# Kernel tuning notes

Hardware: AMD Instinct MI355X
Metric: run time of the kernel (lower is better)

## Reference

```python
import jax, jax.numpy as jnp
import numpy as np

N = 100000      # nodes
E = 3200000     # edges (avg degree 32)
IN = 256        # in_features
OUT = 128       # out_features


def setup_inputs() -> dict:
    key = jax.random.key(0)
    k_x, k_r, k_c, k_v, k_w, k_b = jax.random.split(key, 6)
    x = jax.random.normal(k_x, (N, IN), dtype=jnp.float32)
    row = jax.random.randint(k_r, (E,), 0, N)          # destination node of each edge
    col = jax.random.randint(k_c, (E,), 0, N)          # source node of each edge
    adj_vals = jax.random.uniform(k_v, (E,), dtype=jnp.float32)  # sparse adj values
    stdv = 1.0 / np.sqrt(OUT)                          # matches reset_parameters
    weight = jax.random.uniform(k_w, (IN, OUT), dtype=jnp.float32, minval=-stdv, maxval=stdv)
    bias = jax.random.uniform(k_b, (OUT,), dtype=jnp.float32, minval=-stdv, maxval=stdv)
    return {"x": x, "adj_vals": adj_vals, "weight": weight, "bias": bias,
            "row": row, "col": col}


def reference(x, adj_vals, weight, bias, row, col):
    # support = input @ W                       [N, OUT]
    support = x @ weight
    # output = spmm(adj, support): for each edge (r, c, v): out[r] += v * support[c]
    gathered = adj_vals[:, None] * support[col]  # [E, OUT] irregular gather
    out = jax.ops.segment_sum(gathered, row, num_segments=N)  # [N, OUT] scatter-add
    return out + bias
```

## Files before the change

### kernel.cpp

```cpp
#include <hip/hip_runtime.h>

#define INF 256
#define OUTF 128
#define NBMAX 1024
#define BUCKET_CAP 4608

typedef _Float16 half2v __attribute__((ext_vector_type(2)));
typedef _Float16 half8 __attribute__((ext_vector_type(8)));
typedef float f32x4 __attribute__((ext_vector_type(4)));

__device__ inline unsigned short f16bits(float v) {
    union { unsigned short u; _Float16 h; } cv;
    cv.h = (_Float16)v;
    return cv.u;
}
__device__ inline float f16val15(unsigned rec) {
    union { unsigned short u; _Float16 h; } cv;
    cv.u = (unsigned short)(rec << 1);
    return (float)cv.h;
}

__global__ __launch_bounds__(256) void k_prepack(const float* __restrict__ w,
                                                 _Float16* __restrict__ wpack,
                                                 int* __restrict__ bcursor,
                                                 int NB) {
    int t = blockIdx.x * 256 + threadIdx.x;
    int k = t >> 7, n = t & 127;
    int ks = k >> 5, quad = (k >> 3) & 3, j = k & 7;
    int ct = n >> 4, nn = n & 15;
    wpack[(((ks * 8 + ct) * 4 + quad) * 16 + nn) * 8 + j] = (_Float16)w[k * OUTF + n];
    if (t < NB) bcursor[t] = t * BUCKET_CAP;
}

__global__ __launch_bounds__(256) void gcn_gemm_mfma(const float* __restrict__ x,
                                                     const _Float16* __restrict__ wpack,
                                                     _Float16* __restrict__ support,
                                                     int N) {
    const int tid = threadIdx.x;
    const int wv = tid >> 6;
    const int lane = tid & 63;
    const int m16 = lane & 15;
    const int quad = lane >> 4;
    const int rowbase = blockIdx.x * 128 + wv * 32;

    f32x4 acc[2][8];
#pragma unroll
    for (int rt = 0; rt < 2; ++rt)
#pragma unroll
        for (int ct = 0; ct < 8; ++ct)
            acc[rt][ct] = (f32x4){0.f, 0.f, 0.f, 0.f};

    int r0 = rowbase + m16;
    int r1 = rowbase + 16 + m16;
    int r0c = (r0 < N) ? r0 : N - 1;
    int r1c = (r1 < N) ? r1 : N - 1;
    const float* xr0 = x + (long)r0c * INF + quad * 8;
    const float* xr1 = x + (long)r1c * INF + quad * 8;

    for (int ks = 0; ks < 8; ++ks) {
        float4 u0 = *(const float4*)(xr0 + ks * 32);
        float4 v0 = *(const float4*)(xr0 + ks * 32 + 4);
        float4 u1 = *(const float4*)(xr1 + ks * 32);
        float4 v1 = *(const float4*)(xr1 + ks * 32 + 4);
        half8 a0 = {(_Float16)u0.x, (_Float16)u0.y, (_Float16)u0.z, (_Float16)u0.w,
                    (_Float16)v0.x, (_Float16)v0.y, (_Float16)v0.z, (_Float16)v0.w};
        half8 a1 = {(_Float16)u1.x, (_Float16)u1.y, (_Float16)u1.z, (_Float16)u1.w,
                    (_Float16)v1.x, (_Float16)v1.y, (_Float16)v1.z, (_Float16)v1.w};

        half8 b[8];
#pragma unroll
        for (int ct = 0; ct < 8; ++ct)
            b[ct] = *(const half8*)(wpack + (size_t)(((ks * 8 + ct) * 4 + quad) * 16 + m16) * 8);

#pragma unroll
        for (int ct = 0; ct < 8; ++ct) {
            acc[0][ct] = __builtin_amdgcn_mfma_f32_16x16x32_f16(a0, b[ct], acc[0][ct], 0, 0, 0);
            acc[1][ct] = __builtin_amdgcn_mfma_f32_16x16x32_f16(a1, b[ct], acc[1][ct], 0, 0, 0);
        }
    }

#pragma unroll
    for (int rt = 0; rt < 2; ++rt) {
        int rb = rowbase + rt * 16 + quad * 4;
#pragma unroll
        for (int reg = 0; reg < 4; ++reg) {
            int r = rb + reg;
            if (r < N) {
#pragma unroll
                for (int ct = 0; ct < 8; ++ct)
                    support[(long)r * OUTF + ct * 16 + m16] = (_Float16)acc[rt][ct][reg];
            }
        }
    }
}

__global__ __launch_bounds__(256) void k_coarse_scatter(const int* __restrict__ row,
                                                        const int* __restrict__ col,
                                                        const float* __restrict__ vals,
                                                        int* __restrict__ bcursor,
                                                        uint2* __restrict__ tmp,
                                                        int NB, int E) {
    __shared__ int cnt[NBMAX];
    __shared__ int sbase[NBMAX];
    const int tid = threadIdx.x;
    for (int i = tid; i < NB; i += 256) cnt[i] = 0;
    __syncthreads();

    int b[16], rk[16];
    uint2 rec[16];
    int base = blockIdx.x * 4096;
#pragma unroll
    for (int j = 0; j < 16; ++j) {
        int e = base + j * 256 + tid;
        if (e < E) {
            int r = row[e];
            int c = col[e];
            float v = vals[e];
            rec[j].x = ((unsigned)r << 15) | ((unsigned)f16bits(v) >> 1);
            rec[j].y = (unsigned)c;
            b[j] = r >> 7;
            rk[j] = atomicAdd(&cnt[b[j]], 1);
        } else {
            b[j] = -1;
        }
    }
    __syncthreads();
    for (int i = tid; i < NB; i += 256) {
        int c = cnt[i];
        if (c) sbase[i] = atomicAdd(&bcursor[i], c);
    }
    __syncthreads();
#pragma unroll
    for (int j = 0; j < 16; ++j) {
        if (b[j] >= 0) tmp[sbase[b[j]] + rk[j]] = rec[j];
    }
}

__global__ __launch_bounds__(256) void k_bucket_sort(const uint2* __restrict__ tmp,
                                                     const int* __restrict__ bcursor,
                                                     unsigned* __restrict__ frecs,
                                                     int* __restrict__ rs,
                                                     int* __restrict__ re,
                                                     int N) {
    __shared__ uint2 recs[BUCKET_CAP];
    __shared__ int cnt[128];
    __shared__ int offs[128];

    const int tid = threadIdx.x;
    const int b = blockIdx.x;
    const int start = b * BUCKET_CAP;
    int n = bcursor[b] - start;
    if (n > BUCKET_CAP) n = BUCKET_CAP;
    const int row0 = b << 7;

    if (tid < 128) cnt[tid] = 0;
    __syncthreads();

    for (int i = tid; i < n; i += 256) {
        uint2 r = tmp[start + i];
        recs[i] = r;
        atomicAdd(&cnt[(r.x >> 15) & 127], 1);
    }
    __syncthreads();

    if (tid < 128) offs[tid] = cnt[tid];
    __syncthreads();
    for (int d = 1; d < 128; d <<= 1) {
        int add = 0;
        if (tid < 128 && tid >= d) add = offs[tid - d];
        __syncthreads();
        if (tid < 128) offs[tid] += add;
        __syncthreads();
    }
    if (tid < 128) {
        int excl = offs[tid] - cnt[tid];
        offs[tid] = excl;
        int r = row0 + tid;
        if (r < N) {
            rs[r] = start + excl;
            re[r] = start + excl + cnt[tid];
        }
    }
    __syncthreads();

    for (int i = tid; i < n; i += 256) {
        uint2 r = recs[i];
        int lr = (r.x >> 15) & 127;
        int pos = atomicAdd(&offs[lr], 1);
        frecs[start + pos] = (r.y << 15) | (r.x & 0x7FFF);
    }
}

__global__ __launch_bounds__(256) void k_gather(const half2v* __restrict__ sup,
                                                const unsigned* __restrict__ frecs,
                                                const int* __restrict__ rs,
                                                const int* __restrict__ re,
                                                const float* __restrict__ bias,
                                                float* __restrict__ out,
                                                int N) {
    int wid = (blockIdx.x * 256 + threadIdx.x) >> 6;
    int lane = threadIdx.x & 63;
    if (wid >= N) return;

    int start = rs[wid];
    int end = re[wid];

    float ax = 0.f, ay = 0.f;
    int i = start;
    for (; i + 4 <= end; i += 4) {
        unsigned r0 = frecs[i + 0], r1 = frecs[i + 1];
        unsigned r2 = frecs[i + 2], r3 = frecs[i + 3];
        float v0 = f16val15(r0), v1 = f16val15(r1);
        float v2 = f16val15(r2), v3 = f16val15(r3);
        half2v h0 = sup[(long)(r0 >> 15) * 64 + lane];
        half2v h1 = sup[(long)(r1 >> 15) * 64 + lane];
        half2v h2 = sup[(long)(r2 >> 15) * 64 + lane];
        half2v h3 = sup[(long)(r3 >> 15) * 64 + lane];
        ax += v0 * (float)h0.x + v1 * (float)h1.x + v2 * (float)h2.x + v3 * (float)h3.x;
        ay += v0 * (float)h0.y + v1 * (float)h1.y + v2 * (float)h2.y + v3 * (float)h3.y;
    }
    for (; i < end; ++i) {
        unsigned r = frecs[i];
        float v = f16val15(r);
        half2v h = sup[(long)(r >> 15) * 64 + lane];
        ax += v * (float)h.x;
        ay += v * (float)h.y;
    }

    float2 bb = ((const float2*)bias)[lane];
    float2 o;
    o.x = ax + bb.x;
    o.y = ay + bb.y;
    ((float2*)out)[(long)wid * 64 + lane] = o;
}

extern "C" void kernel_launch(void* const* d_in, const int* in_sizes, int n_in,
                              void* d_out, int out_size, void* d_ws, size_t ws_size,
                              hipStream_t stream) {
    const float* x    = (const float*)d_in[0];
    const float* vals = (const float*)d_in[1];
    const float* w    = (const float*)d_in[2];
    const float* bias = (const float*)d_in[3];
    const int*   row  = (const int*)d_in[4];
    const int*   col  = (const int*)d_in[5];

    const int N = in_sizes[0] / INF;
    const int E = in_sizes[1];
    const int NB = (N + 127) / 128;

    char* p = (char*)d_ws;
    _Float16* support = (_Float16*)p;  p += (size_t)N * OUTF * sizeof(_Float16);
    unsigned* frecs   = (unsigned*)p;  p += (size_t)NB * BUCKET_CAP * sizeof(unsigned);
    _Float16* wpack   = (_Float16*)p;  p += (size_t)INF * OUTF * sizeof(_Float16);
    int* rs           = (int*)p;       p += (size_t)N * sizeof(int);
    int* re           = (int*)p;       p += (size_t)N * sizeof(int);
    int* bcursor      = (int*)p;       p += (size_t)NBMAX * sizeof(int);

    uint2* tmp = (uint2*)d_out;

    const int eb4096 = (E + 4095) / 4096;

    k_prepack<<<(INF * OUTF) / 256, 256, 0, stream>>>(w, wpack, bcursor, NB);

    gcn_gemm_mfma<<<(N + 127) / 128, 256, 0, stream>>>(x, wpack, support, N);

    k_coarse_scatter<<<eb4096, 256, 0, stream>>>(row, col, vals, bcursor, tmp, NB, E);

    k_bucket_sort<<<NB, 256, 0, stream>>>(tmp, bcursor, frecs, rs, re, N);

    {
        int blocks = (N * 64 + 255) / 256;
        k_gather<<<blocks, 256, 0, stream>>>((const half2v*)support, frecs,
                                             rs, re, bias, (float*)d_out, N);
    }
}
```

Before: 408.3 us.

## Merge GEMM and edge scatter into one launch, split-wave gather, drop LDS staging

The GEMM and the coarse edge scatter are independent, so they now run as disjoint block ranges of a single kernel and can overlap on the GPU instead of running back to back. The bucket sort no longer stages records in shared memory and instead re-reads them from global memory, which lowers LDS use and may raise occupancy at the cost of a second global read. The gather splits each wave into two halves that handle alternating edges. Each lane loads 4 halves per edge with vectorized record reads, and the halves are combined by a cross-lane shuffle, which is meant to raise memory-level parallelism.

```diff
diff --git a/kernel.cpp b/kernel.cpp
--- a/kernel.cpp
+++ b/kernel.cpp
@@ -6,6 +6,7 @@
 #define BUCKET_CAP 4608
 
 typedef _Float16 half2v __attribute__((ext_vector_type(2)));
+typedef _Float16 half4 __attribute__((ext_vector_type(4)));
 typedef _Float16 half8 __attribute__((ext_vector_type(8)));
 typedef float f32x4 __attribute__((ext_vector_type(4)));
 
@@ -32,107 +33,108 @@
     if (t < NB) bcursor[t] = t * BUCKET_CAP;
 }
 
-__global__ __launch_bounds__(256) void gcn_gemm_mfma(const float* __restrict__ x,
-                                                     const _Float16* __restrict__ wpack,
-                                                     _Float16* __restrict__ support,
-                                                     int N) {
-    const int tid = threadIdx.x;
-    const int wv = tid >> 6;
-    const int lane = tid & 63;
-    const int m16 = lane & 15;
-    const int quad = lane >> 4;
-    const int rowbase = blockIdx.x * 128 + wv * 32;
-
-    f32x4 acc[2][8];
-#pragma unroll
-    for (int rt = 0; rt < 2; ++rt)
-#pragma unroll
-        for (int ct = 0; ct < 8; ++ct)
-            acc[rt][ct] = (f32x4){0.f, 0.f, 0.f, 0.f};
-
-    int r0 = rowbase + m16;
-    int r1 = rowbase + 16 + m16;
-    int r0c = (r0 < N) ? r0 : N - 1;
-    int r1c = (r1 < N) ? r1 : N - 1;
-    const float* xr0 = x + (long)r0c * INF + quad * 8;
-    const float* xr1 = x + (long)r1c * INF + quad * 8;
-
-    for (int ks = 0; ks < 8; ++ks) {
-        float4 u0 = *(const float4*)(xr0 + ks * 32);
-        float4 v0 = *(const float4*)(xr0 + ks * 32 + 4);
-        float4 u1 = *(const float4*)(xr1 + ks * 32);
-        float4 v1 = *(const float4*)(xr1 + ks * 32 + 4);
-        half8 a0 = {(_Float16)u0.x, (_Float16)u0.y, (_Float16)u0.z, (_Float16)u0.w,
-                    (_Float16)v0.x, (_Float16)v0.y, (_Float16)v0.z, (_Float16)v0.w};
-        half8 a1 = {(_Float16)u1.x, (_Float16)u1.y, (_Float16)u1.z, (_Float16)u1.w,
-                    (_Float16)v1.x, (_Float16)v1.y, (_Float16)v1.z, (_Float16)v1.w};
-
-        half8 b[8];
-#pragma unroll
-        for (int ct = 0; ct < 8; ++ct)
-            b[ct] = *(const half8*)(wpack + (size_t)(((ks * 8 + ct) * 4 + quad) * 16 + m16) * 8);
-
-#pragma unroll
-        for (int ct = 0; ct < 8; ++ct) {
-            acc[0][ct] = __builtin_amdgcn_mfma_f32_16x16x32_f16(a0, b[ct], acc[0][ct], 0, 0, 0);
-            acc[1][ct] = __builtin_amdgcn_mfma_f32_16x16x32_f16(a1, b[ct], acc[1][ct], 0, 0, 0);
-        }
-    }
-
-#pragma unroll
-    for (int rt = 0; rt < 2; ++rt) {
-        int rb = rowbase + rt * 16 + quad * 4;
-#pragma unroll
-        for (int reg = 0; reg < 4; ++reg) {
-            int r = rb + reg;
-            if (r < N) {
-#pragma unroll
-                for (int ct = 0; ct < 8; ++ct)
-                    support[(long)r * OUTF + ct * 16 + m16] = (_Float16)acc[rt][ct][reg];
+__global__ __launch_bounds__(256) void k_gemm_scatter(const float* __restrict__ x,
+                                                      const _Float16* __restrict__ wpack,
+                                                      _Float16* __restrict__ support,
+                                                      int N, int GB,
+                                                      const int* __restrict__ row,
+                                                      const int* __restrict__ col,
+                                                      const float* __restrict__ vals,
+                                                      int* __restrict__ bcursor,
+                                                      uint2* __restrict__ tmp,
+                                                      int NB, int E) {
+    if (blockIdx.x < GB) {
+        const int tid = threadIdx.x;
+        const int wv = tid >> 6;
+        const int lane = tid & 63;
+        const int m16 = lane & 15;
+        const int quad = lane >> 4;
+        const int rowbase = blockIdx.x * 128 + wv * 32;
+
+        f32x4 acc[2][8];
+#pragma unroll
+        for (int rt = 0; rt < 2; ++rt)
+#pragma unroll
+            for (int ct = 0; ct < 8; ++ct)
+                acc[rt][ct] = (f32x4){0.f, 0.f, 0.f, 0.f};
+
+        int r0 = rowbase + m16;
+        int r1 = rowbase + 16 + m16;
+        int r0c = (r0 < N) ? r0 : N - 1;
+        int r1c = (r1 < N) ? r1 : N - 1;
+        const float* xr0 = x + (long)r0c * INF + quad * 8;
+        const float* xr1 = x + (long)r1c * INF + quad * 8;
+
+        for (int ks = 0; ks < 8; ++ks) {
+            float4 u0 = *(const float4*)(xr0 + ks * 32);
+            float4 v0 = *(const float4*)(xr0 + ks * 32 + 4);
+            float4 u1 = *(const float4*)(xr1 + ks * 32);
+            float4 v1 = *(const float4*)(xr1 + ks * 32 + 4);
+            half8 a0 = {(_Float16)u0.x, (_Float16)u0.y, (_Float16)u0.z, (_Float16)u0.w,
+                        (_Float16)v0.x, (_Float16)v0.y, (_Float16)v0.z, (_Float16)v0.w};
+            half8 a1 = {(_Float16)u1.x, (_Float16)u1.y, (_Float16)u1.z, (_Float16)u1.w,
+                        (_Float16)v1.x, (_Float16)v1.y, (_Float16)v1.z, (_Float16)v1.w};
+
+            half8 b[8];
+#pragma unroll
+            for (int ct = 0; ct < 8; ++ct)
+                b[ct] = *(const half8*)(wpack + (size_t)(((ks * 8 + ct) * 4 + quad) * 16 + m16) * 8);
+
+#pragma unroll
+            for (int ct = 0; ct < 8; ++ct) {
+                acc[0][ct] = __builtin_amdgcn_mfma_f32_16x16x32_f16(a0, b[ct], acc[0][ct], 0, 0, 0);
+                acc[1][ct] = __builtin_amdgcn_mfma_f32_16x16x32_f16(a1, b[ct], acc[1][ct], 0, 0, 0);
             }
         }
-    }
-}
-
-__global__ __launch_bounds__(256) void k_coarse_scatter(const int* __restrict__ row,
-                                                        const int* __restrict__ col,
-                                                        const float* __restrict__ vals,
-                                                        int* __restrict__ bcursor,
-                                                        uint2* __restrict__ tmp,
-                                                        int NB, int E) {
-    __shared__ int cnt[NBMAX];
-    __shared__ int sbase[NBMAX];
-    const int tid = threadIdx.x;
-    for (int i = tid; i < NB; i += 256) cnt[i] = 0;
-    __syncthreads();
-
-    int b[16], rk[16];
-    uint2 rec[16];
-    int base = blockIdx.x * 4096;
-#pragma unroll
-    for (int j = 0; j < 16; ++j) {
-        int e = base + j * 256 + tid;
-        if (e < E) {
-            int r = row[e];
-            int c = col[e];
-            float v = vals[e];
-            rec[j].x = ((unsigned)r << 15) | ((unsigned)f16bits(v) >> 1);
-            rec[j].y = (unsigned)c;
-            b[j] = r >> 7;
-            rk[j] = atomicAdd(&cnt[b[j]], 1);
-        } else {
-            b[j] = -1;
-        }
-    }
-    __syncthreads();
-    for (int i = tid; i < NB; i += 256) {
-        int c = cnt[i];
-        if (c) sbase[i] = atomicAdd(&bcursor[i], c);
-    }
-    __syncthreads();
-#pragma unroll
-    for (int j = 0; j < 16; ++j) {
-        if (b[j] >= 0) tmp[sbase[b[j]] + rk[j]] = rec[j];
+
+#pragma unroll
+        for (int rt = 0; rt < 2; ++rt) {
+            int rb = rowbase + rt * 16 + quad * 4;
+#pragma unroll
+            for (int reg = 0; reg < 4; ++reg) {
+                int r = rb + reg;
+                if (r < N) {
+#pragma unroll
+                    for (int ct = 0; ct < 8; ++ct)
+                        support[(long)r * OUTF + ct * 16 + m16] = (_Float16)acc[rt][ct][reg];
+                }
+            }
+        }
+    } else {
+        __shared__ int cnt[NBMAX];
+        __shared__ int sbase[NBMAX];
+        const int tid = threadIdx.x;
+        for (int i = tid; i < NB; i += 256) cnt[i] = 0;
+        __syncthreads();
+
+        int b[16], rk[16];
+        uint2 rec[16];
+        int base = (blockIdx.x - GB) * 4096;
+#pragma unroll
+        for (int j = 0; j < 16; ++j) {
+            int e = base + j * 256 + tid;
+            if (e < E) {
+                int r = row[e];
+                int c = col[e];
+                float v = vals[e];
+                rec[j].x = ((unsigned)r << 15) | ((unsigned)f16bits(v) >> 1);
+                rec[j].y = (unsigned)c;
+                b[j] = r >> 7;
+                rk[j] = atomicAdd(&cnt[b[j]], 1);
+            } else {
+                b[j] = -1;
+            }
+        }
+        __syncthreads();
+        for (int i = tid; i < NB; i += 256) {
+            int c = cnt[i];
+            if (c) sbase[i] = atomicAdd(&bcursor[i], c);
+        }
+        __syncthreads();
+#pragma unroll
+        for (int j = 0; j < 16; ++j) {
+            if (b[j] >= 0) tmp[sbase[b[j]] + rk[j]] = rec[j];
+        }
     }
 }
 
@@ -142,7 +144,6 @@
                                                      int* __restrict__ rs,
                                                      int* __restrict__ re,
                                                      int N) {
-    __shared__ uint2 recs[BUCKET_CAP];
     __shared__ int cnt[128];
     __shared__ int offs[128];
 
@@ -158,7 +159,6 @@
 
     for (int i = tid; i < n; i += 256) {
         uint2 r = tmp[start + i];
-        recs[i] = r;
         atomicAdd(&cnt[(r.x >> 15) & 127], 1);
     }
     __syncthreads();
@@ -184,14 +184,14 @@
     __syncthreads();
 
     for (int i = tid; i < n; i += 256) {
-        uint2 r = recs[i];
+        uint2 r = tmp[start + i];
         int lr = (r.x >> 15) & 127;
         int pos = atomicAdd(&offs[lr], 1);
         frecs[start + pos] = (r.y << 15) | (r.x & 0x7FFF);
     }
 }
 
-__global__ __launch_bounds__(256) void k_gather(const half2v* __restrict__ sup,
+__global__ __launch_bounds__(256) void k_gather(const _Float16* __restrict__ sup,
                                                 const unsigned* __restrict__ frecs,
                                                 const int* __restrict__ rs,
                                                 const int* __restrict__ re,
@@ -202,36 +202,83 @@
     int lane = threadIdx.x & 63;
     if (wid >= N) return;
 
-    int start = rs[wid];
-    int end = re[wid];
-
-    float ax = 0.f, ay = 0.f;
-    int i = start;
-    for (; i + 4 <= end; i += 4) {
-        unsigned r0 = frecs[i + 0], r1 = frecs[i + 1];
-        unsigned r2 = frecs[i + 2], r3 = frecs[i + 3];
-        float v0 = f16val15(r0), v1 = f16val15(r1);
-        float v2 = f16val15(r2), v3 = f16val15(r3);
-        half2v h0 = sup[(long)(r0 >> 15) * 64 + lane];
-        half2v h1 = sup[(long)(r1 >> 15) * 64 + lane];
-        half2v h2 = sup[(long)(r2 >> 15) * 64 + lane];
-        half2v h3 = sup[(long)(r3 >> 15) * 64 + lane];
-        ax += v0 * (float)h0.x + v1 * (float)h1.x + v2 * (float)h2.x + v3 * (float)h3.x;
-        ay += v0 * (float)h0.y + v1 * (float)h1.y + v2 * (float)h2.y + v3 * (float)h3.y;
-    }
-    for (; i < end; ++i) {
+    int i = rs[wid];
+    const int end = re[wid];
+    const int half = lane >> 5;
+    const int fl = lane & 31;
+    const unsigned fboff = (unsigned)fl << 3;
+    const char* supb = (const char*)sup;
+
+    float a0 = 0.f, a1 = 0.f, a2 = 0.f, a3 = 0.f;
+    float b0 = 0.f, b1 = 0.f, b2 = 0.f, b3 = 0.f;
+
+    if (i < end && (i & 1)) {
         unsigned r = frecs[i];
+        float v = half ? 0.f : f16val15(r);
+        half4 h = *(const half4*)(supb + (((r & 0xFFFF8000u) >> 7) + fboff));
+        a0 += v * (float)h.x; a1 += v * (float)h.y;
+        a2 += v * (float)h.z; a3 += v * (float)h.w;
+        ++i;
+    }
+    if (i + 2 <= end && (i & 2)) {
+        uint2 rr = *(const uint2*)(frecs + i);
+        unsigned r = half ? rr.y : rr.x;
         float v = f16val15(r);
-        half2v h = sup[(long)(r >> 15) * 64 + lane];
-        ax += v * (float)h.x;
-        ay += v * (float)h.y;
-    }
-
-    float2 bb = ((const float2*)bias)[lane];
-    float2 o;
-    o.x = ax + bb.x;
-    o.y = ay + bb.y;
-    ((float2*)out)[(long)wid * 64 + lane] = o;
+        half4 h = *(const half4*)(supb + (((r & 0xFFFF8000u) >> 7) + fboff));
+        b0 += v * (float)h.x; b1 += v * (float)h.y;
+        b2 += v * (float)h.z; b3 += v * (float)h.w;
+        i += 2;
+    }
+
+    for (; i + 8 <= end; i += 8) {
+        uint4 rA = *(const uint4*)(frecs + i);
+        uint4 rB = *(const uint4*)(frecs + i + 4);
+        unsigned e0 = half ? rA.y : rA.x;
+        unsigned e1 = half ? rA.w : rA.z;
+        unsigned e2 = half ? rB.y : rB.x;
+        unsigned e3 = half ? rB.w : rB.z;
+        float v0 = f16val15(e0), v1 = f16val15(e1);
+        float v2 = f16val15(e2), v3 = f16val15(e3);
+        half4 h0 = *(const half4*)(supb + (((e0 & 0xFFFF8000u) >> 7) + fboff));
+        half4 h1 = *(const half4*)(supb + (((e1 & 0xFFFF8000u) >> 7) + fboff));
+        half4 h2 = *(const half4*)(supb + (((e2 & 0xFFFF8000u) >> 7) + fboff));
+        half4 h3 = *(const half4*)(supb + (((e3 & 0xFFFF8000u) >> 7) + fboff));
+        a0 += v0 * (float)h0.x; a1 += v0 * (float)h0.y;
+        a2 += v0 * (float)h0.z; a3 += v0 * (float)h0.w;
+        b0 += v1 * (float)h1.x; b1 += v1 * (float)h1.y;
+        b2 += v1 * (float)h1.z; b3 += v1 * (float)h1.w;
+        a0 += v2 * (float)h2.x; a1 += v2 * (float)h2.y;
+        a2 += v2 * (float)h2.z; a3 += v2 * (float)h2.w;
+        b0 += v3 * (float)h3.x; b1 += v3 * (float)h3.y;
+        b2 += v3 * (float)h3.z; b3 += v3 * (float)h3.w;
+    }
+    for (; i + 2 <= end; i += 2) {
+        uint2 rr = *(const uint2*)(frecs + i);
+        unsigned r = half ? rr.y : rr.x;
+        float v = f16val15(r);
+        half4 h = *(const half4*)(supb + (((r & 0xFFFF8000u) >> 7) + fboff));
+        a0 += v * (float)h.x; a1 += v * (float)h.y;
+        a2 += v * (float)h.z; a3 += v * (float)h.w;
+    }
+    if (i < end) {
+        unsigned r = frecs[i];
+        float v = half ? 0.f : f16val15(r);
+        half4 h = *(const half4*)(supb + (((r & 0xFFFF8000u) >> 7) + fboff));
+        a0 += v * (float)h.x; a1 += v * (float)h.y;
+        a2 += v * (float)h.z; a3 += v * (float)h.w;
+    }
+
+    float t0 = a0 + b0, t1 = a1 + b1, t2 = a2 + b2, t3 = a3 + b3;
+    t0 += __shfl_xor(t0, 32);
+    t1 += __shfl_xor(t1, 32);
+    t2 += __shfl_xor(t2, 32);
+    t3 += __shfl_xor(t3, 32);
+
+    if (half == 0) {
+        float4 bb = ((const float4*)bias)[fl];
+        float4 o = {t0 + bb.x, t1 + bb.y, t2 + bb.z, t3 + bb.w};
+        ((float4*)out)[(long)wid * 32 + fl] = o;
+    }
 }
 
 extern "C" void kernel_launch(void* const* d_in, const int* in_sizes, int n_in,
@@ -258,19 +305,18 @@
 
     uint2* tmp = (uint2*)d_out;
 
-    const int eb4096 = (E + 4095) / 4096;
+    const int GB = (N + 127) / 128;
+    const int SB = (E + 4095) / 4096;
 
     k_prepack<<<(INF * OUTF) / 256, 256, 0, stream>>>(w, wpack, bcursor, NB);
 
-    gcn_gemm_mfma<<<(N + 127) / 128, 256, 0, stream>>>(x, wpack, support, N);
-
-    k_coarse_scatter<<<eb4096, 256, 0, stream>>>(row, col, vals, bcursor, tmp, NB, E);
+    k_gemm_scatter<<<GB + SB, 256, 0, stream>>>(x, wpack, support, N, GB,
+                                                row, col, vals, bcursor, tmp, NB, E);
 
     k_bucket_sort<<<NB, 256, 0, stream>>>(tmp, bcursor, frecs, rs, re, N);
 
     {
         int blocks = (N * 64 + 255) / 256;
-        k_gather<<<blocks, 256, 0, stream>>>((const half2v*)support, frecs,
-                                             rs, re, bias, (float*)d_out, N);
-    }
-}
+        k_gather<<<blocks, 256, 0, stream>>>(support, frecs, rs, re, bias, (float*)d_out, N);
+    }
+}
```

After: 393.8 us. 1.04x faster.

## Replace bucket sort with global count-scan-scatter CSR build and vectorized gather

Applied to the files above, without the earlier changes.

Replaces the two-pass coarse-bucket scatter plus per-bucket LDS sort with a per-row atomic count, a two-level prefix scan, and a direct atomic-cursor scatter into exact CSR order. After the scatter the cursor array doubles as row end pointers. The gather kernel now has each quarter-wave handle a different edge, loading 16-byte half8 chunks and reducing across quarters with shuffles. This drops the fixed-capacity bucket overflow risk and the intermediate tmp buffer, at the cost of heavy global atomics on 100k row counters and more kernel launches.

```diff
diff --git a/kernel.cpp b/kernel.cpp
--- a/kernel.cpp
+++ b/kernel.cpp
@@ -2,10 +2,7 @@
 
 #define INF 256
 #define OUTF 128
-#define NBMAX 1024
-#define BUCKET_CAP 4608
-
-typedef _Float16 half2v __attribute__((ext_vector_type(2)));
+
 typedef _Float16 half8 __attribute__((ext_vector_type(8)));
 typedef float f32x4 __attribute__((ext_vector_type(4)));
 
@@ -22,14 +19,15 @@
 
 __global__ __launch_bounds__(256) void k_prepack(const float* __restrict__ w,
                                                  _Float16* __restrict__ wpack,
-                                                 int* __restrict__ bcursor,
-                                                 int NB) {
+                                                 int4* __restrict__ rcnt4,
+                                                 int* __restrict__ bsum) {
     int t = blockIdx.x * 256 + threadIdx.x;
     int k = t >> 7, n = t & 127;
     int ks = k >> 5, quad = (k >> 3) & 3, j = k & 7;
     int ct = n >> 4, nn = n & 15;
     wpack[(((ks * 8 + ct) * 4 + quad) * 16 + nn) * 8 + j] = (_Float16)w[k * OUTF + n];
-    if (t < NB) bcursor[t] = t * BUCKET_CAP;
+    rcnt4[t] = make_int4(0, 0, 0, 0);
+    if (t < 256) bsum[t] = 0;
 }
 
 __global__ __launch_bounds__(256) void gcn_gemm_mfma(const float* __restrict__ x,
@@ -94,104 +92,83 @@
     }
 }
 
-__global__ __launch_bounds__(256) void k_coarse_scatter(const int* __restrict__ row,
-                                                        const int* __restrict__ col,
-                                                        const float* __restrict__ vals,
-                                                        int* __restrict__ bcursor,
-                                                        uint2* __restrict__ tmp,
-                                                        int NB, int E) {
-    __shared__ int cnt[NBMAX];
-    __shared__ int sbase[NBMAX];
-    const int tid = threadIdx.x;
-    for (int i = tid; i < NB; i += 256) cnt[i] = 0;
+__global__ __launch_bounds__(256) void k_count(const int* __restrict__ row,
+                                               int* __restrict__ rcnt, int E) {
+    const int base = blockIdx.x * 4096;
+    const int tid = threadIdx.x;
+#pragma unroll
+    for (int j = 0; j < 16; ++j) {
+        int e = base + j * 256 + tid;
+        if (e < E) atomicAdd(&rcnt[row[e]], 1);
+    }
+}
+
+__global__ __launch_bounds__(256) void k_scan1(const int4* __restrict__ rcnt4,
+                                               int* __restrict__ rs,
+                                               int* __restrict__ bsum) {
+    __shared__ int sd[256];
+    const int tid = threadIdx.x;
+    const int g = blockIdx.x * 256 + tid;
+    int4 c = rcnt4[g];
+    int s = c.x + c.y + c.z + c.w;
+    sd[tid] = s;
     __syncthreads();
-
-    int b[16], rk[16];
-    uint2 rec[16];
-    int base = blockIdx.x * 4096;
+    for (int d = 1; d < 256; d <<= 1) {
+        int t = (tid >= d) ? sd[tid - d] : 0;
+        __syncthreads();
+        sd[tid] += t;
+        __syncthreads();
+    }
+    int excl = sd[tid] - s;
+    int4 o;
+    o.x = excl;
+    o.y = o.x + c.x;
+    o.z = o.y + c.y;
+    o.w = o.z + c.z;
+    ((int4*)rs)[g] = o;
+    if (tid == 255) bsum[blockIdx.x] = sd[255];
+}
+
+__global__ __launch_bounds__(256) void k_scan2(const int* __restrict__ bsum,
+                                               int* __restrict__ rs,
+                                               int* __restrict__ cursor) {
+    __shared__ int ws[4];
+    const int tid = threadIdx.x;
+    const int b = blockIdx.x;
+    int v = (tid < b) ? bsum[tid] : 0;
+#pragma unroll
+    for (int off = 32; off >= 1; off >>= 1) v += __shfl_xor(v, off);
+    if ((tid & 63) == 0) ws[tid >> 6] = v;
+    __syncthreads();
+    int boff = ws[0] + ws[1] + ws[2] + ws[3];
+    int g = b * 256 + tid;
+    int4 r = ((const int4*)rs)[g];
+    r.x += boff; r.y += boff; r.z += boff; r.w += boff;
+    ((int4*)rs)[g] = r;
+    ((int4*)cursor)[g] = r;
+}
+
+__global__ __launch_bounds__(256) void k_scatter(const int* __restrict__ row,
+                                                 const int* __restrict__ col,
+                                                 const float* __restrict__ vals,
+                                                 int* __restrict__ cursor,
+                                                 unsigned* __restrict__ frecs, int E) {
+    const int base = blockIdx.x * 4096;
+    const int tid = threadIdx.x;
 #pragma unroll
     for (int j = 0; j < 16; ++j) {
         int e = base + j * 256 + tid;
         if (e < E) {
             int r = row[e];
-            int c = col[e];
+            unsigned c = (unsigned)col[e];
             float v = vals[e];
-            rec[j].x = ((unsigned)r << 15) | ((unsigned)f16bits(v) >> 1);
-            rec[j].y = (unsigned)c;
-            b[j] = r >> 7;
-            rk[j] = atomicAdd(&cnt[b[j]], 1);
-        } else {
-            b[j] = -1;
-        }
-    }
-    __syncthreads();
-    for (int i = tid; i < NB; i += 256) {
-        int c = cnt[i];
-        if (c) sbase[i] = atomicAdd(&bcursor[i], c);
-    }
-    __syncthreads();
-#pragma unroll
-    for (int j = 0; j < 16; ++j) {
-        if (b[j] >= 0) tmp[sbase[b[j]] + rk[j]] = rec[j];
-    }
-}
-
-__global__ __launch_bounds__(256) void k_bucket_sort(const uint2* __restrict__ tmp,
-                                                     const int* __restrict__ bcursor,
-                                                     unsigned* __restrict__ frecs,
-                                                     int* __restrict__ rs,
-                                                     int* __restrict__ re,
-                                                     int N) {
-    __shared__ uint2 recs[BUCKET_CAP];
-    __shared__ int cnt[128];
-    __shared__ int offs[128];
-
-    const int tid = threadIdx.x;
-    const int b = blockIdx.x;
-    const int start = b * BUCKET_CAP;
-    int n = bcursor[b] - start;
-    if (n > BUCKET_CAP) n = BUCKET_CAP;
-    const int row0 = b << 7;
-
-    if (tid < 128) cnt[tid] = 0;
-    __syncthreads();
-
-    for (int i = tid; i < n; i += 256) {
-        uint2 r = tmp[start + i];
-        recs[i] = r;
-        atomicAdd(&cnt[(r.x >> 15) & 127], 1);
-    }
-    __syncthreads();
-
-    if (tid < 128) offs[tid] = cnt[tid];
-    __syncthreads();
-    for (int d = 1; d < 128; d <<= 1) {
-        int add = 0;
-        if (tid < 128 && tid >= d) add = offs[tid - d];
-        __syncthreads();
-        if (tid < 128) offs[tid] += add;
-        __syncthreads();
-    }
-    if (tid < 128) {
-        int excl = offs[tid] - cnt[tid];
-        offs[tid] = excl;
-        int r = row0 + tid;
-        if (r < N) {
-            rs[r] = start + excl;
-            re[r] = start + excl + cnt[tid];
-        }
-    }
-    __syncthreads();
-
-    for (int i = tid; i < n; i += 256) {
-        uint2 r = recs[i];
-        int lr = (r.x >> 15) & 127;
-        int pos = atomicAdd(&offs[lr], 1);
-        frecs[start + pos] = (r.y << 15) | (r.x & 0x7FFF);
-    }
-}
-
-__global__ __launch_bounds__(256) void k_gather(const half2v* __restrict__ sup,
+            int pos = atomicAdd(&cursor[r], 1);
+            frecs[pos] = (c << 15) | ((unsigned)f16bits(v) >> 1);
+        }
+    }
+}
+
+__global__ __launch_bounds__(256) void k_gather(const _Float16* __restrict__ sup,
                                                 const unsigned* __restrict__ frecs,
                                                 const int* __restrict__ rs,
                                                 const int* __restrict__ re,
@@ -202,36 +179,58 @@
     int lane = threadIdx.x & 63;
     if (wid >= N) return;
 
-    int start = rs[wid];
-    int end = re[wid];
-
-    float ax = 0.f, ay = 0.f;
-    int i = start;
-    for (; i + 4 <= end; i += 4) {
-        unsigned r0 = frecs[i + 0], r1 = frecs[i + 1];
-        unsigned r2 = frecs[i + 2], r3 = frecs[i + 3];
-        float v0 = f16val15(r0), v1 = f16val15(r1);
-        float v2 = f16val15(r2), v3 = f16val15(r3);
-        half2v h0 = sup[(long)(r0 >> 15) * 64 + lane];
-        half2v h1 = sup[(long)(r1 >> 15) * 64 + lane];
-        half2v h2 = sup[(long)(r2 >> 15) * 64 + lane];
-        half2v h3 = sup[(long)(r3 >> 15) * 64 + lane];
-        ax += v0 * (float)h0.x + v1 * (float)h1.x + v2 * (float)h2.x + v3 * (float)h3.x;
-        ay += v0 * (float)h0.y + v1 * (float)h1.y + v2 * (float)h2.y + v3 * (float)h3.y;
-    }
-    for (; i < end; ++i) {
-        unsigned r = frecs[i];
-        float v = f16val15(r);
-        half2v h = sup[(long)(r >> 15) * 64 + lane];
-        ax += v * (float)h.x;
-        ay += v * (float)h.y;
-    }
-
-    float2 bb = ((const float2*)bias)[lane];
-    float2 o;
-    o.x = ax + bb.x;
-    o.y = ay + bb.y;
-    ((float2*)out)[(long)wid * 64 + lane] = o;
+    const int q = lane >> 4;
+    const int fl = lane & 15;
+    const unsigned fb = (unsigned)fl << 4;
+    const char* supb = (const char*)sup;
+
+    int i = rs[wid];
+    const int end = re[wid];
+
+    float a0 = 0.f, a1 = 0.f, a2 = 0.f, a3 = 0.f;
+    float a4 = 0.f, a5 = 0.f, a6 = 0.f, a7 = 0.f;
+
+    for (; i + 16 <= end; i += 16) {
+#pragma unroll
+        for (int k = 0; k < 4; ++k) {
+            unsigned rec = frecs[i + 4 * k + q];
+            float v = f16val15(rec);
+            half8 h = *(const half8*)(supb + (((rec & 0xFFFF8000u) >> 7) + fb));
+            a0 += v * (float)h[0]; a1 += v * (float)h[1];
+            a2 += v * (float)h[2]; a3 += v * (float)h[3];
+            a4 += v * (float)h[4]; a5 += v * (float)h[5];
+            a6 += v * (float)h[6]; a7 += v * (float)h[7];
+        }
+    }
+    for (; i < end; i += 4) {
+        int idx = i + q;
+        unsigned rec = frecs[(idx < end) ? idx : (end - 1)];
+        float v = (idx < end) ? f16val15(rec) : 0.f;
+        half8 h = *(const half8*)(supb + (((rec & 0xFFFF8000u) >> 7) + fb));
+        a0 += v * (float)h[0]; a1 += v * (float)h[1];
+        a2 += v * (float)h[2]; a3 += v * (float)h[3];
+        a4 += v * (float)h[4]; a5 += v * (float)h[5];
+        a6 += v * (float)h[6]; a7 += v * (float)h[7];
+    }
+
+    a0 += __shfl_xor(a0, 16); a0 += __shfl_xor(a0, 32);
+    a1 += __shfl_xor(a1, 16); a1 += __shfl_xor(a1, 32);
+    a2 += __shfl_xor(a2, 16); a2 += __shfl_xor(a2, 32);
+    a3 += __shfl_xor(a3, 16); a3 += __shfl_xor(a3, 32);
+    a4 += __shfl_xor(a4, 16); a4 += __shfl_xor(a4, 32);
+    a5 += __shfl_xor(a5, 16); a5 += __shfl_xor(a5, 32);
+    a6 += __shfl_xor(a6, 16); a6 += __shfl_xor(a6, 32);
+    a7 += __shfl_xor(a7, 16); a7 += __shfl_xor(a7, 32);
+
+    if (q == 0) {
+        float4 b0 = ((const float4*)bias)[fl * 2];
+        float4 b1 = ((const float4*)bias)[fl * 2 + 1];
+        float4 o0 = {a0 + b0.x, a1 + b0.y, a2 + b0.z, a3 + b0.w};
+        float4 o1 = {a4 + b1.x, a5 + b1.y, a6 + b1.z, a7 + b1.w};
+        float4* orow = (float4*)(out + (long)wid * OUTF);
+        orow[fl * 2] = o0;
+        orow[fl * 2 + 1] = o1;
+    }
 }
 
 extern "C" void kernel_launch(void* const* d_in, const int* in_sizes, int n_in,
@@ -246,31 +245,33 @@
 
     const int N = in_sizes[0] / INF;
     const int E = in_sizes[1];
-    const int NB = (N + 127) / 128;
+    const int SB1 = (N + 1023) / 1024;
 
     char* p = (char*)d_ws;
     _Float16* support = (_Float16*)p;  p += (size_t)N * OUTF * sizeof(_Float16);
-    unsigned* frecs   = (unsigned*)p;  p += (size_t)NB * BUCKET_CAP * sizeof(unsigned);
+    unsigned* frecs   = (unsigned*)p;  p += (size_t)E * sizeof(unsigned);
     _Float16* wpack   = (_Float16*)p;  p += (size_t)INF * OUTF * sizeof(_Float16);
-    int* rs           = (int*)p;       p += (size_t)N * sizeof(int);
-    int* re           = (int*)p;       p += (size_t)N * sizeof(int);
-    int* bcursor      = (int*)p;       p += (size_t)NBMAX * sizeof(int);
-
-    uint2* tmp = (uint2*)d_out;
-
-    const int eb4096 = (E + 4095) / 4096;
-
-    k_prepack<<<(INF * OUTF) / 256, 256, 0, stream>>>(w, wpack, bcursor, NB);
+    int* rcnt         = (int*)p;       p += (size_t)131072 * sizeof(int);
+    int* rs           = (int*)p;       p += (size_t)SB1 * 1024 * sizeof(int);
+    int* cursor       = (int*)p;       p += (size_t)SB1 * 1024 * sizeof(int);
+    int* bsum         = (int*)p;       p += 256 * sizeof(int);
+
+    const int EB = (E + 4095) / 4096;
+
+    k_prepack<<<(INF * OUTF) / 256, 256, 0, stream>>>(w, wpack, (int4*)rcnt, bsum);
 
     gcn_gemm_mfma<<<(N + 127) / 128, 256, 0, stream>>>(x, wpack, support, N);
 
-    k_coarse_scatter<<<eb4096, 256, 0, stream>>>(row, col, vals, bcursor, tmp, NB, E);
-
-    k_bucket_sort<<<NB, 256, 0, stream>>>(tmp, bcursor, frecs, rs, re, N);
+    k_count<<<EB, 256, 0, stream>>>(row, rcnt, E);
+
+    k_scan1<<<SB1, 256, 0, stream>>>((const int4*)rcnt, rs, bsum);
+    k_scan2<<<SB1, 256, 0, stream>>>(bsum, rs, cursor);
+
+    k_scatter<<<EB, 256, 0, stream>>>(row, col, vals, cursor, frecs, E);
 
     {
         int blocks = (N * 64 + 255) / 256;
-        k_gather<<<blocks, 256, 0, stream>>>((const half2v*)support, frecs,
-                                             rs, re, bias, (float*)d_out, N);
-    }
-}
+        k_gather<<<blocks, 256, 0, stream>>>(support, frecs, rs, cursor, bias,
+                                             (float*)d_out, N);
+    }
+}
```

After: 656.4 us. +60.8%, slower.

## Widen row buckets to 512, drop LDS staging in sort, vectorize gather loads

Applied to the files above, without the earlier changes.

Coarse buckets now cover 512 rows instead of 128, which gives fewer buckets (at most 196) and fewer global atomics on bucket cursors. The bucket sort runs with 512 threads and no longer stages records in shared memory. It reads tmp twice from global memory instead, which frees LDS for higher occupancy. The gather kernel splits each wave into 4 groups of 16 lanes, and each lane loads 16-byte half8 chunks so 4 edges are processed in parallel; partial sums are combined with cross-lane shuffles. This trades more gather memory-level parallelism for extra shuffle work and larger per-bucket capacity assumptions.

```diff
diff --git a/kernel.cpp b/kernel.cpp
--- a/kernel.cpp
+++ b/kernel.cpp
@@ -2,10 +2,10 @@
 
 #define INF 256
 #define OUTF 128
-#define NBMAX 1024
-#define BUCKET_CAP 4608
-
-typedef _Float16 half2v __attribute__((ext_vector_type(2)));
+#define RB 512
+#define NBMAX 256
+#define BUCKET_CAP 17408
+
 typedef _Float16 half8 __attribute__((ext_vector_type(8)));
 typedef float f32x4 __attribute__((ext_vector_type(4)));
 
@@ -103,7 +103,7 @@
     __shared__ int cnt[NBMAX];
     __shared__ int sbase[NBMAX];
     const int tid = threadIdx.x;
-    for (int i = tid; i < NB; i += 256) cnt[i] = 0;
+    if (tid < NB) cnt[tid] = 0;
     __syncthreads();
 
     int b[16], rk[16];
@@ -118,16 +118,16 @@
             float v = vals[e];
             rec[j].x = ((unsigned)r << 15) | ((unsigned)f16bits(v) >> 1);
             rec[j].y = (unsigned)c;
-            b[j] = r >> 7;
+            b[j] = r >> 9;
             rk[j] = atomicAdd(&cnt[b[j]], 1);
         } else {
             b[j] = -1;
         }
     }
     __syncthreads();
-    for (int i = tid; i < NB; i += 256) {
-        int c = cnt[i];
-        if (c) sbase[i] = atomicAdd(&bcursor[i], c);
+    if (tid < NB) {
+        int c = cnt[tid];
+        if (c) sbase[tid] = atomicAdd(&bcursor[tid], c);
     }
     __syncthreads();
 #pragma unroll
@@ -136,43 +136,40 @@
     }
 }
 
-__global__ __launch_bounds__(256) void k_bucket_sort(const uint2* __restrict__ tmp,
+__global__ __launch_bounds__(512) void k_bucket_sort(const uint2* __restrict__ tmp,
                                                      const int* __restrict__ bcursor,
                                                      unsigned* __restrict__ frecs,
                                                      int* __restrict__ rs,
                                                      int* __restrict__ re,
                                                      int N) {
-    __shared__ uint2 recs[BUCKET_CAP];
-    __shared__ int cnt[128];
-    __shared__ int offs[128];
+    __shared__ int cnt[RB];
+    __shared__ int offs[RB];
 
     const int tid = threadIdx.x;
     const int b = blockIdx.x;
     const int start = b * BUCKET_CAP;
     int n = bcursor[b] - start;
     if (n > BUCKET_CAP) n = BUCKET_CAP;
-    const int row0 = b << 7;
-
-    if (tid < 128) cnt[tid] = 0;
-    __syncthreads();
-
-    for (int i = tid; i < n; i += 256) {
+    const int row0 = b * RB;
+
+    cnt[tid] = 0;
+    __syncthreads();
+
+    for (int i = tid; i < n; i += 512) {
         uint2 r = tmp[start + i];
-        recs[i] = r;
-        atomicAdd(&cnt[(r.x >> 15) & 127], 1);
-    }
-    __syncthreads();
-
-    if (tid < 128) offs[tid] = cnt[tid];
-    __syncthreads();
-    for (int d = 1; d < 128; d <<= 1) {
-        int add = 0;
-        if (tid < 128 && tid >= d) add = offs[tid - d];
+        atomicAdd(&cnt[(r.x >> 15) & (RB - 1)], 1);
+    }
+    __syncthreads();
+
+    offs[tid] = cnt[tid];
+    __syncthreads();
+    for (int d = 1; d < RB; d <<= 1) {
+        int add = (tid >= d) ? offs[tid - d] : 0;
         __syncthreads();
-        if (tid < 128) offs[tid] += add;
+        offs[tid] += add;
         __syncthreads();
     }
-    if (tid < 128) {
+    {
         int excl = offs[tid] - cnt[tid];
         offs[tid] = excl;
         int r = row0 + tid;
@@ -183,15 +180,15 @@
     }
     __syncthreads();
 
-    for (int i = tid; i < n; i += 256) {
-        uint2 r = recs[i];
-        int lr = (r.x >> 15) & 127;
+    for (int i = tid; i < n; i += 512) {
+        uint2 r = tmp[start + i];
+        int lr = (r.x >> 15) & (RB - 1);
         int pos = atomicAdd(&offs[lr], 1);
         frecs[start + pos] = (r.y << 15) | (r.x & 0x7FFF);
     }
 }
 
-__global__ __launch_bounds__(256) void k_gather(const half2v* __restrict__ sup,
+__global__ __launch_bounds__(256) void k_gather(const _Float16* __restrict__ sup,
                                                 const unsigned* __restrict__ frecs,
                                                 const int* __restrict__ rs,
                                                 const int* __restrict__ re,
@@ -202,36 +199,58 @@
     int lane = threadIdx.x & 63;
     if (wid >= N) return;
 
-    int start = rs[wid];
-    int end = re[wid];
-
-    float ax = 0.f, ay = 0.f;
-    int i = start;
-    for (; i + 4 <= end; i += 4) {
-        unsigned r0 = frecs[i + 0], r1 = frecs[i + 1];
-        unsigned r2 = frecs[i + 2], r3 = frecs[i + 3];
-        float v0 = f16val15(r0), v1 = f16val15(r1);
-        float v2 = f16val15(r2), v3 = f16val15(r3);
-        half2v h0 = sup[(long)(r0 >> 15) * 64 + lane];
-        half2v h1 = sup[(long)(r1 >> 15) * 64 + lane];
-        half2v h2 = sup[(long)(r2 >> 15) * 64 + lane];
-        half2v h3 = sup[(long)(r3 >> 15) * 64 + lane];
-        ax += v0 * (float)h0.x + v1 * (float)h1.x + v2 * (float)h2.x + v3 * (float)h3.x;
-        ay += v0 * (float)h0.y + v1 * (float)h1.y + v2 * (float)h2.y + v3 * (float)h3.y;
-    }
-    for (; i < end; ++i) {
-        unsigned r = frecs[i];
-        float v = f16val15(r);
-        half2v h = sup[(long)(r >> 15) * 64 + lane];
-        ax += v * (float)h.x;
-        ay += v * (float)h.y;
-    }
-
-    float2 bb = ((const float2*)bias)[lane];
-    float2 o;
-    o.x = ax + bb.x;
-    o.y = ay + bb.y;
-    ((float2*)out)[(long)wid * 64 + lane] = o;
+    const int q = lane >> 4;
+    const int fl = lane & 15;
+    const unsigned fb = (unsigned)fl << 4;
+    const char* supb = (const char*)sup;
+
+    int i = rs[wid];
+    const int end = re[wid];
+
+    float a0 = 0.f, a1 = 0.f, a2 = 0.f, a3 = 0.f;
+    float a4 = 0.f, a5 = 0.f, a6 = 0.f, a7 = 0.f;
+
+    for (; i + 16 <= end; i += 16) {
+#pragma unroll
+        for (int k = 0; k < 4; ++k) {
+            unsigned rec = frecs[i + 4 * k + q];
+            float v = f16val15(rec);
+            half8 h = *(const half8*)(supb + (((rec & 0xFFFF8000u) >> 7) + fb));
+            a0 += v * (float)h[0]; a1 += v * (float)h[1];
+            a2 += v * (float)h[2]; a3 += v * (float)h[3];
+            a4 += v * (float)h[4]; a5 += v * (float)h[5];
+            a6 += v * (float)h[6]; a7 += v * (float)h[7];
+        }
+    }
+    for (; i < end; i += 4) {
+        int idx = i + q;
+        unsigned rec = frecs[(idx < end) ? idx : (end - 1)];
+        float v = (idx < end) ? f16val15(rec) : 0.f;
+        half8 h = *(const half8*)(supb + (((rec & 0xFFFF8000u) >> 7) + fb));
+        a0 += v * (float)h[0]; a1 += v * (float)h[1];
+        a2 += v * (float)h[2]; a3 += v * (float)h[3];
+        a4 += v * (float)h[4]; a5 += v * (float)h[5];
+        a6 += v * (float)h[6]; a7 += v * (float)h[7];
+    }
+
+    a0 += __shfl_xor(a0, 16); a0 += __shfl_xor(a0, 32);
+    a1 += __shfl_xor(a1, 16); a1 += __shfl_xor(a1, 32);
+    a2 += __shfl_xor(a2, 16); a2 += __shfl_xor(a2, 32);
+    a3 += __shfl_xor(a3, 16); a3 += __shfl_xor(a3, 32);
+    a4 += __shfl_xor(a4, 16); a4 += __shfl_xor(a4, 32);
+    a5 += __shfl_xor(a5, 16); a5 += __shfl_xor(a5, 32);
+    a6 += __shfl_xor(a6, 16); a6 += __shfl_xor(a6, 32);
+    a7 += __shfl_xor(a7, 16); a7 += __shfl_xor(a7, 32);
+
+    if (q == 0) {
+        float4 b0 = ((const float4*)bias)[fl * 2];
+        float4 b1 = ((const float4*)bias)[fl * 2 + 1];
+        float4 o0 = {a0 + b0.x, a1 + b0.y, a2 + b0.z, a3 + b0.w};
+        float4 o1 = {a4 + b1.x, a5 + b1.y, a6 + b1.z, a7 + b1.w};
+        float4* orow = (float4*)(out + (long)wid * OUTF);
+        orow[fl * 2] = o0;
+        orow[fl * 2 + 1] = o1;
+    }
 }
 
 extern "C" void kernel_launch(void* const* d_in, const int* in_sizes, int n_in,
@@ -246,7 +265,7 @@
 
     const int N = in_sizes[0] / INF;
     const int E = in_sizes[1];
-    const int NB = (N + 127) / 128;
+    const int NB = (N + RB - 1) / RB;
 
     char* p = (char*)d_ws;
     _Float16* support = (_Float16*)p;  p += (size_t)N * OUTF * sizeof(_Float16);
@@ -258,19 +277,19 @@
 
     uint2* tmp = (uint2*)d_out;
 
-    const int eb4096 = (E + 4095) / 4096;
+    const int EB = (E + 4095) / 4096;
 
     k_prepack<<<(INF * OUTF) / 256, 256, 0, stream>>>(w, wpack, bcursor, NB);
 
     gcn_gemm_mfma<<<(N + 127) / 128, 256, 0, stream>>>(x, wpack, support, N);
 
-    k_coarse_scatter<<<eb4096, 256, 0, stream>>>(row, col, vals, bcursor, tmp, NB, E);
-
-    k_bucket_sort<<<NB, 256, 0, stream>>>(tmp, bcursor, frecs, rs, re, N);
+    k_coarse_scatter<<<EB, 256, 0, stream>>>(row, col, vals, bcursor, tmp, NB, E);
+
+    k_bucket_sort<<<NB, 512, 0, stream>>>(tmp, bcursor, frecs, rs, re, N);
 
     {
         int blocks = (N * 64 + 255) / 256;
-        k_gather<<<blocks, 256, 0, stream>>>((const half2v*)support, frecs,
-                                             rs, re, bias, (float*)d_out, N);
-    }
-}
+        k_gather<<<blocks, 256, 0, stream>>>(support, frecs, rs, re, bias,
+                                             (float*)d_out, N);
+    }
+}
```

Result: faster. 381.8 us (-6.5%).
